# Performance work log

Hardware: AMD Instinct MI355X
Metric: run time of the kernel (lower is better)

## Reference

```python
import jax, jax.numpy as jnp
import numpy as np

N = 50000      # nodes
E = 600000     # edges
P = 200000     # prediction edges
IN = 128       # in_channels
HID = 128      # hidden per head
H1, H2 = 4, 2  # heads
BN_EPS = 1e-5
NEG_SLOPE = 0.2


def _rn(k, shape, scale=0.05):
    return jax.random.normal(k, shape, jnp.float32) * scale


def setup_inputs() -> dict:
    key = jax.random.key(0)
    ks = jax.random.split(key, 24)
    inp = {}
    inp['x'] = jax.random.normal(ks[0], (N, IN), jnp.float32)
    inp['ei'] = jax.random.randint(ks[1], (2, E), 0, N, dtype=jnp.int32)
    inp['pred_edges'] = jax.random.randint(ks[2], (2, P), 0, N, dtype=jnp.int32)
    inp['pert'] = jax.random.normal(ks[3], (N,), jnp.float32)
    inp['pr'] = jax.random.uniform(ks[4], (N,), jnp.float32)
    # GATv2 layer 1: in=IN -> H1 heads x HID
    inp['Wl1'] = _rn(ks[5], (IN, H1 * HID))
    inp['bl1'] = jnp.zeros((H1 * HID,), jnp.float32)
    inp['Wr1'] = _rn(ks[6], (IN, H1 * HID))
    inp['br1'] = jnp.zeros((H1 * HID,), jnp.float32)
    inp['att1'] = _rn(ks[7], (H1, HID))
    inp['bias1'] = jnp.zeros((H1 * HID,), jnp.float32)
    # BatchNorm1d(H1*HID) eval-mode params
    inp['bn1_g'] = jnp.ones((H1 * HID,), jnp.float32)
    inp['bn1_b'] = jnp.zeros((H1 * HID,), jnp.float32)
    inp['bn1_m'] = _rn(ks[8], (H1 * HID,))
    inp['bn1_v'] = jax.random.uniform(ks[9], (H1 * HID,), jnp.float32, 0.5, 1.5)
    # GATv2 layer 2: in=H1*HID -> H2 heads x HID
    inp['Wl2'] = _rn(ks[10], (H1 * HID, H2 * HID))
    inp['bl2'] = jnp.zeros((H2 * HID,), jnp.float32)
    inp['Wr2'] = _rn(ks[11], (H1 * HID, H2 * HID))
    inp['br2'] = jnp.zeros((H2 * HID,), jnp.float32)
    inp['att2'] = _rn(ks[12], (H2, HID))
    inp['bias2'] = jnp.zeros((H2 * HID,), jnp.float32)
    inp['bn2_g'] = jnp.ones((H2 * HID,), jnp.float32)
    inp['bn2_b'] = jnp.zeros((H2 * HID,), jnp.float32)
    inp['bn2_m'] = _rn(ks[13], (H2 * HID,))
    inp['bn2_v'] = jax.random.uniform(ks[14], (H2 * HID,), jnp.float32, 0.5, 1.5)
    # proj: Linear(H2*HID*2 + 2 + 1, 2)
    inp['Wp'] = _rn(ks[15], (H2 * HID * 2 + 3, 2))
    inp['bp'] = jnp.zeros((2,), jnp.float32)
    return inp


def gatv2(x, src, dst, Wl, bl, Wr, br, att, bias, n):
    """GATv2Conv (concat=True): e_ij = att . LeakyReLU(xl_j + xr_i), segment softmax over dst."""
    H, C = att.shape
    xl = (x @ Wl + bl).reshape(n, H, C)
    xr = (x @ Wr + br).reshape(n, H, C)
    e = jax.nn.leaky_relu(xl[src] + xr[dst], NEG_SLOPE)     # [E, H, C]
    score = jnp.einsum('ehc,hc->eh', e, att)                 # [E, H]
    m = jax.ops.segment_max(score, dst, num_segments=n)     # [N, H]
    ex = jnp.exp(score - m[dst])
    denom = jax.ops.segment_sum(ex, dst, num_segments=n)
    alpha = ex / denom[dst]                                  # [E, H]
    out = jax.ops.segment_sum(alpha[:, :, None] * xl[src], dst, num_segments=n)
    return out.reshape(n, H * C) + bias


def batchnorm_eval(h, g, b, m, v):
    return (h - m) * jax.lax.rsqrt(v + BN_EPS) * g + b


def reference(x, ei, pred_edges, pert, pr,
              Wl1, bl1, Wr1, br1, att1, bias1, bn1_g, bn1_b, bn1_m, bn1_v,
              Wl2, bl2, Wr2, br2, att2, bias2, bn2_g, bn2_b, bn2_m, bn2_v,
              Wp, bp):
    n = x.shape[0]
    loop = jnp.arange(n, dtype=ei.dtype)                    # add_self_loops=True
    src = jnp.concatenate([ei[0], loop])
    dst = jnp.concatenate([ei[1], loop])
    h = gatv2(x, src, dst, Wl1, bl1, Wr1, br1, att1, bias1, n)
    h = jax.nn.relu(batchnorm_eval(h, bn1_g, bn1_b, bn1_m, bn1_v))
    h = gatv2(h, src, dst, Wl2, bl2, Wr2, br2, att2, bias2, n)
    z = jax.nn.relu(batchnorm_eval(h, bn2_g, bn2_b, bn2_m, bn2_v))
    s, d = pred_edges[0], pred_edges[1]
    feat = jnp.concatenate([z[s], z[d], pr[s][:, None], pr[d][:, None],
                            (pert[s] * pert[d])[:, None]], axis=1)
    return feat @ Wp + bp
```

## Files before the change

kernel.cpp:

```cpp
#include <hip/hip_runtime.h>
#include <math.h>

#define BN_EPS 1e-5f
#define N_NODES 50000
#define E_EDGES 600000

typedef __attribute__((ext_vector_type(8))) short bf16x8;
typedef __attribute__((ext_vector_type(4))) short bf16x4;
typedef __attribute__((ext_vector_type(4))) float f32x4;

__device__ __forceinline__ short f2bf(float f) {
    unsigned u = __float_as_uint(f);
    u += 0x7fffu + ((u >> 16) & 1u);
    return (short)(u >> 16);
}
__device__ __forceinline__ float bf2f(short s) {
    return __uint_as_float(((unsigned)(unsigned short)s) << 16);
}

__device__ short g_xlb[(size_t)N_NODES * 512];
__device__ short g_xrb[(size_t)N_NODES * 512];
__device__ short g_h1b[(size_t)N_NODES * 512];
__device__ short g_xb[(size_t)N_NODES * 128];
__device__ float g_zf[(size_t)N_NODES * 256];
__device__ short g_wt[393216];
__device__ int   g_rowptr[N_NODES + 1];
__device__ int   g_bsum[256];
__device__ int   g_cursor[N_NODES];
__device__ int   g_counts[N_NODES];
__device__ int   g_csrc[E_EDGES + N_NODES];


__global__ void k_init_counts(int* __restrict__ counts, int n) {
    int i = blockIdx.x * blockDim.x + threadIdx.x;
    if (i < n) counts[i] = 1;
}

__global__ void k_hist(const int* __restrict__ ei, int E, int* __restrict__ counts) {
    int e = blockIdx.x * blockDim.x + threadIdx.x;
    if (e < E) atomicAdd(&counts[ei[E + e]], 1);
}

__global__ void k_scan1(const int* __restrict__ counts, int n,
                        int* __restrict__ rp, int* __restrict__ bsum) {
    __shared__ int sd[256];
    int t = threadIdx.x;
    int g = blockIdx.x * 256 + t;
    int v = (g < n) ? counts[g] : 0;
    sd[t] = v;
    __syncthreads();
    for (int o = 1; o < 256; o <<= 1) {
        int u = (t >= o) ? sd[t - o] : 0;
        __syncthreads();
        sd[t] += u;
        __syncthreads();
    }
    if (g < n) rp[g + 1] = sd[t];
    if (t == 255) bsum[blockIdx.x] = sd[255];
}

__global__ void k_scan2(int* __restrict__ bsum, int nb) {
    __shared__ int sd[256];
    int t = threadIdx.x;
    int v = (t < nb) ? bsum[t] : 0;
    sd[t] = v;
    __syncthreads();
    for (int o = 1; o < 256; o <<= 1) {
        int u = (t >= o) ? sd[t - o] : 0;
        __syncthreads();
        sd[t] += u;
        __syncthreads();
    }
    if (t < nb) bsum[t] = sd[t] - v;
}

__global__ void k_scan3(int* __restrict__ rp, const int* __restrict__ bsum, int n) {
    int g = blockIdx.x * blockDim.x + threadIdx.x;
    if (g < n) rp[g + 1] += bsum[g >> 8];
    if (g == 0) rp[0] = 0;
}

__global__ void k_fill(const int* __restrict__ rp, int* __restrict__ cursor,
                       int* __restrict__ csrc, int n) {
    int i = blockIdx.x * blockDim.x + threadIdx.x;
    if (i < n) {
        int p = rp[i];
        csrc[p] = i;
        cursor[i] = p + 1;
    }
}

__global__ void k_scatter(const int* __restrict__ ei, int E,
                          int* __restrict__ cursor, int* __restrict__ csrc) {
    int e = blockIdx.x * blockDim.x + threadIdx.x;
    if (e < E) {
        int d = ei[E + e];
        int p = atomicAdd(&cursor[d], 1);
        csrc[p] = ei[e];
    }
}


__global__ void k_f32_to_bf16_v4(const float* __restrict__ in, short* __restrict__ out,
                                 int n4) {
    int i = blockIdx.x * blockDim.x + threadIdx.x;
    if (i < n4) {
        float4 v = ((const float4*)in)[i];
        short4 o;
        o.x = f2bf(v.x); o.y = f2bf(v.y); o.z = f2bf(v.z); o.w = f2bf(v.w);
        ((short4*)out)[i] = o;
    }
}

__global__ void k_transpose_w(const float* __restrict__ W, short* __restrict__ Wt,
                              int K, int N) {
    __shared__ float s[32][33];
    int n0 = blockIdx.x * 32, k0 = blockIdx.y * 32;
    int tx = threadIdx.x, ty = threadIdx.y;
    #pragma unroll
    for (int q = 0; q < 4; q++)
        s[ty * 4 + q][tx] = W[(size_t)(k0 + ty * 4 + q) * N + n0 + tx];
    __syncthreads();
    #pragma unroll
    for (int q = 0; q < 4; q++)
        Wt[(size_t)(n0 + ty * 4 + q) * K + k0 + tx] = f2bf(s[tx][ty * 4 + q]);
}

__global__ __launch_bounds__(256) void k_gemm_mfma(
    const short* __restrict__ A, const short* __restrict__ Bt,
    const float* __restrict__ bias, short* __restrict__ C,
    int M, int N, int K)
{
    __shared__ short sA[128][72];
    __shared__ short sB[128][72];
    int tid = threadIdx.x;
    int wid = tid >> 6, lane = tid & 63;
    int m0 = blockIdx.y * 128, n0 = blockIdx.x * 128;
    int wr = (wid >> 1) * 64;
    int wc = (wid & 1) * 64;
    f32x4 acc[4][4] = {};

    for (int k0 = 0; k0 < K; k0 += 64) {
        #pragma unroll
        for (int i = 0; i < 4; i++) {
            int c = tid + i * 256;
            int r = c >> 3;
            int col = (c & 7) * 8;
            bf16x8 v = {};
            int gr = m0 + r;
            if (gr < M) v = *(const bf16x8*)(A + (size_t)gr * K + k0 + col);
            *(bf16x8*)&sA[r][col] = v;
        }
        #pragma unroll
        for (int i = 0; i < 4; i++) {
            int c = tid + i * 256;
            int r = c >> 3;
            int col = (c & 7) * 8;
            bf16x8 v = *(const bf16x8*)(Bt + (size_t)(n0 + r) * K + k0 + col);
            *(bf16x8*)&sB[r][col] = v;
        }
        __syncthreads();
        #pragma unroll
        for (int kk = 0; kk < 2; kk++) {
            bf16x8 af[4], bfr[4];
            #pragma unroll
            for (int i = 0; i < 4; i++)
                af[i] = *(bf16x8*)&sA[wr + i * 16 + (lane & 15)][kk * 32 + (lane >> 4) * 8];
            #pragma unroll
            for (int j = 0; j < 4; j++)
                bfr[j] = *(bf16x8*)&sB[wc + j * 16 + (lane & 15)][kk * 32 + (lane >> 4) * 8];
            #pragma unroll
            for (int i = 0; i < 4; i++)
                #pragma unroll
                for (int j = 0; j < 4; j++)
                    acc[i][j] = __builtin_amdgcn_mfma_f32_16x16x32_bf16(
                        af[i], bfr[j], acc[i][j], 0, 0, 0);
        }
        __syncthreads();
    }
    #pragma unroll
    for (int i = 0; i < 4; i++) {
        #pragma unroll
        for (int j = 0; j < 4; j++) {
            int colg = n0 + wc + j * 16 + (lane & 15);
            float b = bias[colg];
            #pragma unroll
            for (int q = 0; q < 4; q++) {
                int rowg = m0 + wr + i * 16 + (lane >> 4) * 4 + q;
                if (rowg < M) C[(size_t)rowg * N + colg] = f2bf(acc[i][j][q] + b);
            }
        }
    }
}

template <int H, typename OT>
__global__ void k_gat_agg(const short* __restrict__ xl, const short* __restrict__ xr,
                          const float* __restrict__ att,
                          const int* __restrict__ rp, const int* __restrict__ csrc,
                          const float* __restrict__ bias,
                          const float* __restrict__ bng, const float* __restrict__ bnb,
                          const float* __restrict__ bnm, const float* __restrict__ bnv,
                          OT* __restrict__ out, int n) {
    constexpr int G = 64 / H;
    constexpr int CPL = 128 / G;
    const int D = H * 128;
    int wid = (blockIdx.x * blockDim.x + threadIdx.x) >> 6;
    int lane = threadIdx.x & 63;
    if (wid >= n) return;
    const int i = wid;
    const int h = lane / G;
    const int ch0 = h * 128 + (lane % G) * CPL;

    float xrv[CPL], attv[CPL];
    {
        short raw[CPL];
        if constexpr (CPL == 8)
            *(bf16x8*)raw = *(const bf16x8*)(xr + (size_t)i * D + ch0);
        else
            *(bf16x4*)raw = *(const bf16x4*)(xr + (size_t)i * D + ch0);
        #pragma unroll
        for (int q = 0; q < CPL; q++) {
            xrv[q] = bf2f(raw[q]);
            attv[q] = att[ch0 + q];
        }
    }
    float m = -INFINITY, dnm = 0.f, acc[CPL] = {};

    int e0 = rp[i], e1 = rp[i + 1];
    for (int e = e0; e < e1; e++) {
        int j = csrc[e];
        float xlv[CPL];
        {
            short raw[CPL];
            if constexpr (CPL == 8)
                *(bf16x8*)raw = *(const bf16x8*)(xl + (size_t)j * D + ch0);
            else
                *(bf16x4*)raw = *(const bf16x4*)(xl + (size_t)j * D + ch0);
            #pragma unroll
            for (int q = 0; q < CPL; q++) xlv[q] = bf2f(raw[q]);
        }
        float part = 0.f;
        #pragma unroll
        for (int q = 0; q < CPL; q++) {
            float v = xlv[q] + xrv[q];
            v = fmaxf(v, 0.2f * v);
            part = fmaf(attv[q], v, part);
        }
        #pragma unroll
        for (int o = G / 2; o > 0; o >>= 1) part += __shfl_xor(part, o, 64);
        float mn = fmaxf(m, part);
        float scale = __expf(m - mn);
        float p = __expf(part - mn);
        dnm = dnm * scale + p;
        #pragma unroll
        for (int q = 0; q < CPL; q++) acc[q] = fmaf(p, xlv[q], acc[q] * scale);
        m = mn;
    }

    float inv = 1.f / dnm;
    float res[CPL];
    #pragma unroll
    for (int q = 0; q < CPL; q++) {
        int ch = ch0 + q;
        float o = acc[q] * inv + bias[ch];
        float vv = (o - bnm[ch]) * rsqrtf(bnv[ch] + BN_EPS) * bng[ch] + bnb[ch];
        res[q] = fmaxf(vv, 0.f);
    }
    if constexpr (sizeof(OT) == 2) {
        short ov[CPL];
        #pragma unroll
        for (int q = 0; q < CPL; q++) ov[q] = f2bf(res[q]);
        if constexpr (CPL == 8)
            *(bf16x8*)(out + (size_t)i * D + ch0) = *(bf16x8*)ov;
        else
            *(bf16x4*)(out + (size_t)i * D + ch0) = *(bf16x4*)ov;
    } else {
        if constexpr (CPL == 4) {
            *(float4*)((float*)out + (size_t)i * D + ch0) =
                make_float4(res[0], res[1], res[2], res[3]);
        } else {
            #pragma unroll
            for (int q = 0; q < CPL; q++) out[(size_t)i * D + ch0 + q] = res[q];
        }
    }
}

__global__ void k_pred(const float* __restrict__ z, const int* __restrict__ pe,
                       const float* __restrict__ pr, const float* __restrict__ pert,
                       const float* __restrict__ Wp, const float* __restrict__ bp,
                       float* __restrict__ out, int P) {
    int wid = (blockIdx.x * blockDim.x + threadIdx.x) >> 6;
    int lane = threadIdx.x & 63;
    if (wid >= P) return;
    int s = pe[wid], d = pe[P + wid];
    float4 zs = *(const float4*)(z + (size_t)s * 256 + lane * 4);
    float4 zd = *(const float4*)(z + (size_t)d * 256 + lane * 4);
    float a0 = 0.f, a1 = 0.f;
    const float* zsp = (const float*)&zs;
    const float* zdp = (const float*)&zd;
    #pragma unroll
    for (int q = 0; q < 4; q++) {
        int f1 = lane * 4 + q;
        int f2 = 256 + lane * 4 + q;
        a0 += zsp[q] * Wp[f1 * 2 + 0] + zdp[q] * Wp[f2 * 2 + 0];
        a1 += zsp[q] * Wp[f1 * 2 + 1] + zdp[q] * Wp[f2 * 2 + 1];
    }
    #pragma unroll
    for (int o = 32; o > 0; o >>= 1) {
        a0 += __shfl_xor(a0, o, 64);
        a1 += __shfl_xor(a1, o, 64);
    }
    if (lane == 0) {
        float prs = pr[s], prd = pr[d], pp = pert[s] * pert[d];
        a0 += prs * Wp[512 * 2 + 0] + prd * Wp[513 * 2 + 0] + pp * Wp[514 * 2 + 0] + bp[0];
        a1 += prs * Wp[512 * 2 + 1] + prd * Wp[513 * 2 + 1] + pp * Wp[514 * 2 + 1] + bp[1];
        *(float2*)(out + (size_t)wid * 2) = make_float2(a0, a1);
    }
}


extern "C" void kernel_launch(void* const* d_in, const int* in_sizes, int n_in,
                              void* d_out, int out_size, void* d_ws, size_t ws_size,
                              hipStream_t stream) {
    const float* x    = (const float*)d_in[0];
    const int*   ei   = (const int*)d_in[1];
    const int*   pe   = (const int*)d_in[2];
    const float* pert = (const float*)d_in[3];
    const float* pr   = (const float*)d_in[4];
    const float* Wl1  = (const float*)d_in[5];
    const float* bl1  = (const float*)d_in[6];
    const float* Wr1  = (const float*)d_in[7];
    const float* br1  = (const float*)d_in[8];
    const float* att1 = (const float*)d_in[9];
    const float* bias1= (const float*)d_in[10];
    const float* bn1g = (const float*)d_in[11];
    const float* bn1b = (const float*)d_in[12];
    const float* bn1m = (const float*)d_in[13];
    const float* bn1v = (const float*)d_in[14];
    const float* Wl2  = (const float*)d_in[15];
    const float* bl2  = (const float*)d_in[16];
    const float* Wr2  = (const float*)d_in[17];
    const float* br2  = (const float*)d_in[18];
    const float* att2 = (const float*)d_in[19];
    const float* bias2= (const float*)d_in[20];
    const float* bn2g = (const float*)d_in[21];
    const float* bn2b = (const float*)d_in[22];
    const float* bn2m = (const float*)d_in[23];
    const float* bn2v = (const float*)d_in[24];
    const float* Wp   = (const float*)d_in[25];
    const float* bp   = (const float*)d_in[26];

    const int n  = in_sizes[3];
    const int E  = in_sizes[1] / 2;
    const int P  = in_sizes[2] / 2;
    const int IN = in_sizes[0] / n;
    const int D1 = 512, D2 = 256;

    static short* xlb = nullptr;
    static short* xrb = nullptr;
    static short* h1b = nullptr;
    static short* xb  = nullptr;
    static float* zf  = nullptr;
    static short* wt  = nullptr;
    static int *rowptr = nullptr, *bsum = nullptr, *cursor = nullptr,
               *counts = nullptr, *csrc = nullptr;
    if (!xlb) {
        hipGetSymbolAddress((void**)&xlb,    HIP_SYMBOL(g_xlb));
        hipGetSymbolAddress((void**)&xrb,    HIP_SYMBOL(g_xrb));
        hipGetSymbolAddress((void**)&h1b,    HIP_SYMBOL(g_h1b));
        hipGetSymbolAddress((void**)&xb,     HIP_SYMBOL(g_xb));
        hipGetSymbolAddress((void**)&zf,     HIP_SYMBOL(g_zf));
        hipGetSymbolAddress((void**)&wt,     HIP_SYMBOL(g_wt));
        hipGetSymbolAddress((void**)&rowptr, HIP_SYMBOL(g_rowptr));
        hipGetSymbolAddress((void**)&bsum,   HIP_SYMBOL(g_bsum));
        hipGetSymbolAddress((void**)&cursor, HIP_SYMBOL(g_cursor));
        hipGetSymbolAddress((void**)&counts, HIP_SYMBOL(g_counts));
        hipGetSymbolAddress((void**)&csrc,   HIP_SYMBOL(g_csrc));
    }

    short* xl1b = xlb;
    short* xr1b = xrb;
    short* xl2b = xlb;
    short* xr2b = xlb + (size_t)n * D2;
    short* Wl1t = wt;
    short* Wr1t = wt + 65536;
    short* Wl2t = wt + 131072;
    short* Wr2t = wt + 262144;

    const int nb = (n + 255) / 256;

    k_init_counts<<<nb, 256, 0, stream>>>(counts, n);
    k_hist<<<(E + 255) / 256, 256, 0, stream>>>(ei, E, counts);
    k_scan1<<<nb, 256, 0, stream>>>(counts, n, rowptr, bsum);
    k_scan2<<<1, 256, 0, stream>>>(bsum, nb);
    k_scan3<<<nb, 256, 0, stream>>>(rowptr, bsum, n);
    k_fill<<<nb, 256, 0, stream>>>(rowptr, cursor, csrc, n);
    k_scatter<<<(E + 255) / 256, 256, 0, stream>>>(ei, E, cursor, csrc);

    {
        int n4 = n * IN / 4;
        k_f32_to_bf16_v4<<<(n4 + 255) / 256, 256, 0, stream>>>(x, xb, n4);
        k_transpose_w<<<dim3(D1 / 32, IN / 32), dim3(32, 8), 0, stream>>>(Wl1, Wl1t, IN, D1);
        k_transpose_w<<<dim3(D1 / 32, IN / 32), dim3(32, 8), 0, stream>>>(Wr1, Wr1t, IN, D1);
        k_transpose_w<<<dim3(D2 / 32, D1 / 32), dim3(32, 8), 0, stream>>>(Wl2, Wl2t, D1, D2);
        k_transpose_w<<<dim3(D2 / 32, D1 / 32), dim3(32, 8), 0, stream>>>(Wr2, Wr2t, D1, D2);
    }

    const int mb = (n + 127) / 128;

    k_gemm_mfma<<<dim3(D1 / 128, mb), 256, 0, stream>>>(xb, Wl1t, bl1, xl1b, n, D1, IN);
    k_gemm_mfma<<<dim3(D1 / 128, mb), 256, 0, stream>>>(xb, Wr1t, br1, xr1b, n, D1, IN);
    k_gat_agg<4, short><<<(n + 3) / 4, 256, 0, stream>>>(xl1b, xr1b, att1, rowptr, csrc,
                                                  bias1, bn1g, bn1b, bn1m, bn1v, h1b, n);
    k_gemm_mfma<<<dim3(D2 / 128, mb), 256, 0, stream>>>(h1b, Wl2t, bl2, xl2b, n, D2, D1);
    k_gemm_mfma<<<dim3(D2 / 128, mb), 256, 0, stream>>>(h1b, Wr2t, br2, xr2b, n, D2, D1);
    k_gat_agg<2, float><<<(n + 3) / 4, 256, 0, stream>>>(xl2b, xr2b, att2, rowptr, csrc,
                                                  bias2, bn2g, bn2b, bn2m, bn2v, zf, n);
    k_pred<<<(P + 3) / 4, 256, 0, stream>>>(zf, pe, pr, pert, Wp, bp,
                                            (float*)d_out, P);
}
```

Measured before the change: 669.7 us.

## Fuse left/right GEMMs into one dual-output kernel and unroll edge aggregation by two

The separate Wl and Wr projection GEMMs become a single kernel whose block computes a 128x256 tile over the concatenated transposed weights. The A tile is loaded once and feeds both halves, and the epilogue routes the output to xl or xr. This cuts A-operand reloads and launches. The GAT aggregation loop now handles two edges per iteration with a combined online-softmax update, which adds memory-level parallelism on the gathers. The cost is more accumulator registers (32 f32x4) and larger shared memory per block, which may lower occupancy. LDS row padding also changes from 72 to 68, which could affect bank conflicts.

```diff
diff --git a/kernel.cpp b/kernel.cpp
--- a/kernel.cpp
+++ b/kernel.cpp
@@ -126,19 +126,23 @@
         Wt[(size_t)(n0 + ty * 4 + q) * K + k0 + tx] = f2bf(s[tx][ty * 4 + q]);
 }
 
-__global__ __launch_bounds__(256) void k_gemm_mfma(
+__global__ __launch_bounds__(256) void k_gemm_dual(
     const short* __restrict__ A, const short* __restrict__ Bt,
-    const float* __restrict__ bias, short* __restrict__ C,
+    const float* __restrict__ bias_l, const float* __restrict__ bias_r,
+    short* __restrict__ Cl, short* __restrict__ Cr,
     int M, int N, int K)
 {
-    __shared__ short sA[128][72];
-    __shared__ short sB[128][72];
+    __shared__ short sA[128][68];
+    __shared__ short sB0[128][68];
+    __shared__ short sB1[128][68];
     int tid = threadIdx.x;
     int wid = tid >> 6, lane = tid & 63;
-    int m0 = blockIdx.y * 128, n0 = blockIdx.x * 128;
+    int m0 = blockIdx.y * 128;
+    int n0 = blockIdx.x * 256;
     int wr = (wid >> 1) * 64;
     int wc = (wid & 1) * 64;
-    f32x4 acc[4][4] = {};
+    f32x4 acc0[4][4] = {};
+    f32x4 acc1[4][4] = {};
 
     for (int k0 = 0; k0 < K; k0 += 64) {
         #pragma unroll
@@ -150,44 +154,55 @@
             int gr = m0 + r;
             if (gr < M) v = *(const bf16x8*)(A + (size_t)gr * K + k0 + col);
             *(bf16x8*)&sA[r][col] = v;
-        }
-        #pragma unroll
-        for (int i = 0; i < 4; i++) {
-            int c = tid + i * 256;
-            int r = c >> 3;
-            int col = (c & 7) * 8;
-            bf16x8 v = *(const bf16x8*)(Bt + (size_t)(n0 + r) * K + k0 + col);
-            *(bf16x8*)&sB[r][col] = v;
+            bf16x8 b0 = *(const bf16x8*)(Bt + (size_t)(n0 + r) * K + k0 + col);
+            *(bf16x8*)&sB0[r][col] = b0;
+            bf16x8 b1 = *(const bf16x8*)(Bt + (size_t)(n0 + 128 + r) * K + k0 + col);
+            *(bf16x8*)&sB1[r][col] = b1;
         }
         __syncthreads();
         #pragma unroll
         for (int kk = 0; kk < 2; kk++) {
-            bf16x8 af[4], bfr[4];
+            bf16x8 af[4], bf0[4], bf1[4];
             #pragma unroll
             for (int i = 0; i < 4; i++)
                 af[i] = *(bf16x8*)&sA[wr + i * 16 + (lane & 15)][kk * 32 + (lane >> 4) * 8];
             #pragma unroll
-            for (int j = 0; j < 4; j++)
-                bfr[j] = *(bf16x8*)&sB[wc + j * 16 + (lane & 15)][kk * 32 + (lane >> 4) * 8];
+            for (int j = 0; j < 4; j++) {
+                bf0[j] = *(bf16x8*)&sB0[wc + j * 16 + (lane & 15)][kk * 32 + (lane >> 4) * 8];
+                bf1[j] = *(bf16x8*)&sB1[wc + j * 16 + (lane & 15)][kk * 32 + (lane >> 4) * 8];
+            }
             #pragma unroll
             for (int i = 0; i < 4; i++)
                 #pragma unroll
-                for (int j = 0; j < 4; j++)
-                    acc[i][j] = __builtin_amdgcn_mfma_f32_16x16x32_bf16(
-                        af[i], bfr[j], acc[i][j], 0, 0, 0);
-        }
-        __syncthreads();
-    }
+                for (int j = 0; j < 4; j++) {
+                    acc0[i][j] = __builtin_amdgcn_mfma_f32_16x16x32_bf16(
+                        af[i], bf0[j], acc0[i][j], 0, 0, 0);
+                    acc1[i][j] = __builtin_amdgcn_mfma_f32_16x16x32_bf16(
+                        af[i], bf1[j], acc1[i][j], 0, 0, 0);
+                }
+        }
+        __syncthreads();
+    }
+    short* outp;
+    const float* bp2;
+    int cb;
+    if (n0 < N) { outp = Cl; bp2 = bias_l; cb = n0; }
+    else        { outp = Cr; bp2 = bias_r; cb = n0 - N; }
     #pragma unroll
     for (int i = 0; i < 4; i++) {
         #pragma unroll
         for (int j = 0; j < 4; j++) {
-            int colg = n0 + wc + j * 16 + (lane & 15);
-            float b = bias[colg];
+            int c0 = cb + wc + j * 16 + (lane & 15);
+            int c1 = c0 + 128;
+            float b0 = bp2[c0];
+            float b1 = bp2[c1];
             #pragma unroll
             for (int q = 0; q < 4; q++) {
                 int rowg = m0 + wr + i * 16 + (lane >> 4) * 4 + q;
-                if (rowg < M) C[(size_t)rowg * N + colg] = f2bf(acc[i][j][q] + b);
+                if (rowg < M) {
+                    outp[(size_t)rowg * N + c0] = f2bf(acc0[i][j][q] + b0);
+                    outp[(size_t)rowg * N + c1] = f2bf(acc1[i][j][q] + b1);
+                }
             }
         }
     }
@@ -227,7 +242,48 @@
     float m = -INFINITY, dnm = 0.f, acc[CPL] = {};
 
     int e0 = rp[i], e1 = rp[i + 1];
-    for (int e = e0; e < e1; e++) {
+    int e = e0;
+    for (; e + 1 < e1; e += 2) {
+        int j0 = csrc[e], j1 = csrc[e + 1];
+        float xlv0[CPL], xlv1[CPL];
+        {
+            short r0[CPL], r1[CPL];
+            if constexpr (CPL == 8) {
+                *(bf16x8*)r0 = *(const bf16x8*)(xl + (size_t)j0 * D + ch0);
+                *(bf16x8*)r1 = *(const bf16x8*)(xl + (size_t)j1 * D + ch0);
+            } else {
+                *(bf16x4*)r0 = *(const bf16x4*)(xl + (size_t)j0 * D + ch0);
+                *(bf16x4*)r1 = *(const bf16x4*)(xl + (size_t)j1 * D + ch0);
+            }
+            #pragma unroll
+            for (int q = 0; q < CPL; q++) { xlv0[q] = bf2f(r0[q]); xlv1[q] = bf2f(r1[q]); }
+        }
+        float p0 = 0.f, p1 = 0.f;
+        #pragma unroll
+        for (int q = 0; q < CPL; q++) {
+            float v0 = xlv0[q] + xrv[q];
+            float v1 = xlv1[q] + xrv[q];
+            v0 = fmaxf(v0, 0.2f * v0);
+            v1 = fmaxf(v1, 0.2f * v1);
+            p0 = fmaf(attv[q], v0, p0);
+            p1 = fmaf(attv[q], v1, p1);
+        }
+        #pragma unroll
+        for (int o = G / 2; o > 0; o >>= 1) {
+            p0 += __shfl_xor(p0, o, 64);
+            p1 += __shfl_xor(p1, o, 64);
+        }
+        float mn = fmaxf(m, fmaxf(p0, p1));
+        float scale = __expf(m - mn);
+        float w0 = __expf(p0 - mn);
+        float w1 = __expf(p1 - mn);
+        dnm = dnm * scale + w0 + w1;
+        #pragma unroll
+        for (int q = 0; q < CPL; q++)
+            acc[q] = fmaf(w1, xlv1[q], fmaf(w0, xlv0[q], acc[q] * scale));
+        m = mn;
+    }
+    if (e < e1) {
         int j = csrc[e];
         float xlv[CPL];
         {
@@ -382,6 +438,8 @@
     short* xr1b = xrb;
     short* xl2b = xlb;
     short* xr2b = xlb + (size_t)n * D2;
+    short* WtL1 = wt;
+    short* WtL2 = wt + 131072;
     short* Wl1t = wt;
     short* Wr1t = wt + 65536;
     short* Wl2t = wt + 131072;
@@ -408,12 +466,12 @@
 
     const int mb = (n + 127) / 128;
 
-    k_gemm_mfma<<<dim3(D1 / 128, mb), 256, 0, stream>>>(xb, Wl1t, bl1, xl1b, n, D1, IN);
-    k_gemm_mfma<<<dim3(D1 / 128, mb), 256, 0, stream>>>(xb, Wr1t, br1, xr1b, n, D1, IN);
+    k_gemm_dual<<<dim3(2 * D1 / 256, mb), 256, 0, stream>>>(
+        xb, WtL1, bl1, br1, xl1b, xr1b, n, D1, IN);
     k_gat_agg<4, short><<<(n + 3) / 4, 256, 0, stream>>>(xl1b, xr1b, att1, rowptr, csrc,
                                                   bias1, bn1g, bn1b, bn1m, bn1v, h1b, n);
-    k_gemm_mfma<<<dim3(D2 / 128, mb), 256, 0, stream>>>(h1b, Wl2t, bl2, xl2b, n, D2, D1);
-    k_gemm_mfma<<<dim3(D2 / 128, mb), 256, 0, stream>>>(h1b, Wr2t, br2, xr2b, n, D2, D1);
+    k_gemm_dual<<<dim3(2 * D2 / 256, mb), 256, 0, stream>>>(
+        h1b, WtL2, bl2, br2, xl2b, xr2b, n, D2, D1);
     k_gat_agg<2, float><<<(n + 3) / 4, 256, 0, stream>>>(xl2b, xr2b, att2, rowptr, csrc,
                                                   bias2, bn2g, bn2b, bn2m, bn2v, zf, n);
     k_pred<<<(P + 3) / 4, 256, 0, stream>>>(zf, pe, pr, pert, Wp, bp,
```

After: 638.4 us. -4.7%, faster.
